# Kernel tuning notes

Measured on AMD Instinct MI355X. Metric: run time of the kernel, lower is better.

The kernel has to match this reference:

```python
import jax, jax.numpy as jnp
import numpy as np

K = 32        # max neighbors per query point
RADIUS = 0.1  # ball radius
N1 = 8192
N2 = 8192


def setup_inputs() -> dict:
    key = jax.random.key(0)
    k1, k2 = jax.random.split(key)
    points1 = jax.random.uniform(k1, (1, N1, 3), dtype=jnp.float32)
    points2 = jax.random.uniform(k2, (1, N2, 3), dtype=jnp.float32)
    lengths1 = jnp.full((1,), N1, dtype=jnp.int32)  # unused by the kernel, kept for API parity
    lengths2 = jnp.full((1,), N2, dtype=jnp.int32)
    return {"points1": points1, "points2": points2, "lengths1": lengths1, "lengths2": lengths2}


def _ball_query(p1, p2, k, radius):
    # p1: [N1,3], p2: [N2,3]
    # squared distances via gram trick, no [N1,N2,3] diff tensor
    d2 = (jnp.sum(p1 * p1, axis=-1)[:, None]
          + jnp.sum(p2 * p2, axis=-1)[None, :]
          - 2.0 * (p1 @ p2.T))                                   # [N1,N2]
    within = d2 <= radius * radius                                # kernel skips only if dist > radius
    n2 = p2.shape[0]
    # pick the first k in-range neighbors in index order (deterministic stand-in
    # for the unspecified hash-grid traversal order)
    score = jnp.where(within, jnp.arange(n2, dtype=jnp.int32), n2)  # [N1,N2]
    _, idx = jax.lax.top_k(-score, k)                             # k smallest scores -> first k indices
    valid = jnp.take_along_axis(within, idx, axis=1)              # [N1,k]
    counts = jnp.minimum(jnp.sum(within, axis=-1), k).astype(jnp.int32)  # [N1]
    mapping = jnp.where(valid, idx, 0).astype(jnp.int32)          # zeros-padded like the torch buffer
    outputs = jnp.where(valid[..., None], p2[mapping], 0.0)       # [N1,k,3]
    return mapping, counts, outputs


def reference(points1, points2, lengths1, lengths2):
    mapping, num_neighbors, outputs = _ball_query(points1[0], points2[0], K, RADIUS)
    return mapping[None], num_neighbors[None], outputs[None]
```

## Files before the change

kernel.cpp:

```cpp
#include <hip/hip_runtime.h>

#define N1 8192
#define N2 8192
#define KNN 32
#define R2_F32 0.009999999776482582f

#define GDIM 10
#define NCELLS (GDIM * GDIM * GDIM)
#define CELL_W 0.109375f
#define INV_W  9.142857142857142f
#define CAP 40
#define HCAP 128
#define PRUNE2 0.0105f

#define WS_CNT 0
#define WS_PTS 4096

__device__ __forceinline__ int cell_coord(float v) {
    int c = (int)(v * INV_W);
    return c > (GDIM - 1) ? (GDIM - 1) : c;
}

__device__ __forceinline__ int prefix_lt(unsigned long long m) {
    return (int)__builtin_amdgcn_mbcnt_hi(
        (unsigned)(m >> 32),
        __builtin_amdgcn_mbcnt_lo((unsigned)m, 0u));
}

__global__ __launch_bounds__(256) void k_scatter(const float* __restrict__ p2,
                                                 int* __restrict__ cnt,
                                                 float4* __restrict__ pts) {
    const int j = (int)(blockIdx.x * blockDim.x + threadIdx.x);
    if (j < N2) {
        const float x = p2[3 * j], y = p2[3 * j + 1], z = p2[3 * j + 2];
        const int c = (cell_coord(x) * GDIM + cell_coord(y)) * GDIM + cell_coord(z);
        const int slot = atomicAdd(&cnt[c], 1);
        if (slot < CAP) pts[c * CAP + slot] = make_float4(x, y, z, (float)j);
    }
}

__global__ __launch_bounds__(256) void k_query(
    const float* __restrict__ p1, const float4* __restrict__ pts,
    const int* __restrict__ cnt,
    float* __restrict__ map_f, float* __restrict__ cnt_f, float* __restrict__ out_f)
{
    __shared__ float4 hits[4][HCAP];
    __shared__ int cum_l[4][32];
    __shared__ int adj_l[4][32];
    const int w    = (int)(threadIdx.x >> 6);
    const int lane = (int)(threadIdx.x & 63);
    const int q    = (int)blockIdx.x * 4 + w;

    const float qx = p1[3 * q], qy = p1[3 * q + 1], qz = p1[3 * q + 2];
    const float s1 = __fadd_rn(__fadd_rn(__fmul_rn(qx, qx), __fmul_rn(qy, qy)),
                               __fmul_rn(qz, qz));

    const int cx = cell_coord(qx), cy = cell_coord(qy), cz = cell_coord(qz);

    int len = 0, id = 0;
    if (lane < 27) {
        const int ax = cx + lane / 9 - 1;
        const int ay = cy + (lane / 3) % 3 - 1;
        const int az = cz + lane % 3 - 1;
        const bool valid = (unsigned)ax < GDIM && (unsigned)ay < GDIM && (unsigned)az < GDIM;
        if (valid) {
            id = (ax * GDIM + ay) * GDIM + az;
            const float gx = fmaxf(0.0f, fmaxf((float)ax * CELL_W - qx, qx - (float)(ax + 1) * CELL_W));
            const float gy = fmaxf(0.0f, fmaxf((float)ay * CELL_W - qy, qy - (float)(ay + 1) * CELL_W));
            const float gz = fmaxf(0.0f, fmaxf((float)az * CELL_W - qz, qz - (float)(az + 1) * CELL_W));
            const float mind2 = gx * gx + gy * gy + gz * gz;
            if (mind2 <= PRUNE2) {
                int c = cnt[id];
                len = c < CAP ? c : CAP;
            }
        }
    }

    int cum = len;
#pragma unroll
    for (int d = 1; d < 32; d <<= 1) {
        const int v = __shfl_up(cum, d, 64);
        if (lane >= d) cum += v;
    }
    const int T = __shfl(cum, 26, 64);
    if (lane < 32) {
        cum_l[w][lane] = cum;
        adj_l[w][lane] = id * CAP - (cum - len);
    }

    int hcnt = 0;
    for (int g0 = 0; g0 < T; g0 += 64) {
        const int g = g0 + lane;
        const bool active = g < T;
        int lo = 0;
#pragma unroll
        for (int st = 16; st > 0; st >>= 1)
            if (cum_l[w][lo + st - 1] <= g) lo += st;
        float4 e = make_float4(2.0f, 2.0f, 2.0f, 0.0f);
        if (active) e = pts[g + adj_l[w][lo]];
        const float s2  = __fadd_rn(__fadd_rn(__fmul_rn(e.x, e.x), __fmul_rn(e.y, e.y)),
                                    __fmul_rn(e.z, e.z));
        const float dot = __fmaf_rn(qz, e.z, __fmaf_rn(qy, e.y, __fmul_rn(qx, e.x)));
        const float d2  = __fsub_rn(__fadd_rn(s1, s2), __fadd_rn(dot, dot));
        const bool within = active && (d2 <= R2_F32);
        const unsigned long long m = __ballot(within);
        if (m) {
            const int pos = hcnt + prefix_lt(m);
            if (within && pos < HCAP) hits[w][pos] = e;
            hcnt += (int)__popcll(m);
        }
    }

    const int cap = hcnt < HCAP ? hcnt : HCAP;
    int k0 = 0x7FFFFFFF, k1 = 0x7FFFFFFF;
    if (lane < cap)      k0 = (((int)hits[w][lane].w) << 7) | lane;
    if (lane + 64 < cap) k1 = (((int)hits[w][lane + 64].w) << 7) | (lane + 64);
    for (int k = 2; k <= 128; k <<= 1) {
        for (int s = k >> 1; s > 0; s >>= 1) {
            if (s == 64) {
                const int lo2 = k0 < k1 ? k0 : k1;
                const int hi2 = k0 < k1 ? k1 : k0;
                k0 = lo2; k1 = hi2;
            } else {
                const int p0 = __shfl_xor(k0, s, 64);
                const int p1 = __shfl_xor(k1, s, 64);
                const bool lower = (lane & s) == 0;
                const bool asc0  = ((lane     ) & k) == 0;
                const bool asc1  = ((lane + 64) & k) == 0;
                k0 = (lower == asc0) ? (k0 < p0 ? k0 : p0) : (k0 > p0 ? k0 : p0);
                k1 = (lower == asc1) ? (k1 < p1 ? k1 : p1) : (k1 > p1 ? k1 : p1);
            }
        }
    }

    const int outc = hcnt < KNN ? hcnt : KNN;
    if (lane < KNN) {
        const int s = q * KNN + lane;
        float* o = out_f + s * 3;
        if (lane < outc) {
            const float4 e = hits[w][k0 & 127];
            map_f[s] = (float)(k0 >> 7);
            o[0] = e.x; o[1] = e.y; o[2] = e.z;
        } else {
            map_f[s] = 0.0f;
            o[0] = 0.0f; o[1] = 0.0f; o[2] = 0.0f;
        }
    }
    if (lane == 0) cnt_f[q] = (float)outc;
}

extern "C" void kernel_launch(void* const* d_in, const int* in_sizes, int n_in,
                              void* d_out, int out_size, void* d_ws, size_t ws_size,
                              hipStream_t stream) {
    const float* p1 = (const float*)d_in[0];
    const float* p2 = (const float*)d_in[1];
    float* out = (float*)d_out;

    float* map_f = out;
    float* cnt_f = out + (size_t)N1 * KNN;
    float* out_f = cnt_f + N1;

    char* ws = (char*)d_ws;
    int*    cnt = (int*)(ws + WS_CNT);
    float4* pts = (float4*)(ws + WS_PTS);

    hipMemsetAsync(cnt, 0, NCELLS * sizeof(int), stream);
    hipLaunchKernelGGL(k_scatter, dim3(N2 / 256), dim3(256), 0, stream, p2, cnt, pts);
    hipLaunchKernelGGL(k_query,   dim3(N1 / 4),   dim3(256), 0, stream,
                       p1, pts, cnt, map_f, cnt_f, out_f);
}
```

Before: 23.76 us.

## Replace atomic scatter and memset with per-cell gather build kernel

Grid construction changes from an atomic scatter over points (which needs a memset first) to one block per cell. Each block scans all of points2 and compacts the points that fall in its cell with ballots, in index order. This drops the memset launch and the atomics, and makes cell contents deterministic and index-ordered. The cost is redundant work: every one of the 1000 blocks reads all 8192 points, about 1000x the global reads of the old scatter, though those reads likely hit in cache.

```diff
diff --git a/kernel.cpp b/kernel.cpp
--- a/kernel.cpp
+++ b/kernel.cpp
@@ -16,6 +16,16 @@
 #define WS_CNT 0
 #define WS_PTS 4096
 
+struct F3 { float x, y, z; };
+
+__device__ __forceinline__ F3 ld3(const float* __restrict__ p, int j) {
+    F3 r;
+    r.x = p[3 * j + 0];
+    r.y = p[3 * j + 1];
+    r.z = p[3 * j + 2];
+    return r;
+}
+
 __device__ __forceinline__ int cell_coord(float v) {
     int c = (int)(v * INV_W);
     return c > (GDIM - 1) ? (GDIM - 1) : c;
@@ -27,16 +37,64 @@
         __builtin_amdgcn_mbcnt_lo((unsigned)m, 0u));
 }
 
-__global__ __launch_bounds__(256) void k_scatter(const float* __restrict__ p2,
-                                                 int* __restrict__ cnt,
-                                                 float4* __restrict__ pts) {
-    const int j = (int)(blockIdx.x * blockDim.x + threadIdx.x);
-    if (j < N2) {
-        const float x = p2[3 * j], y = p2[3 * j + 1], z = p2[3 * j + 2];
-        const int c = (cell_coord(x) * GDIM + cell_coord(y)) * GDIM + cell_coord(z);
-        const int slot = atomicAdd(&cnt[c], 1);
-        if (slot < CAP) pts[c * CAP + slot] = make_float4(x, y, z, (float)j);
-    }
+__global__ __launch_bounds__(256) void k_build(const float* __restrict__ p2,
+                                               int* __restrict__ cnt,
+                                               float4* __restrict__ pts) {
+    __shared__ float4 buf[4][CAP];
+    __shared__ int    cl[4];
+    const int w    = (int)(threadIdx.x >> 6);
+    const int lane = (int)(threadIdx.x & 63);
+    const int c    = (int)blockIdx.x;
+    const int ccx = c / 100, ccy = (c / 10) % 10, ccz = c % 10;
+
+    int count = 0;
+    const int jofs = w * (N2 / 4);
+
+    auto proc = [&](const F3& p, int jb) {
+        const bool match = (cell_coord(p.x) == ccx) &&
+                           (cell_coord(p.y) == ccy) &&
+                           (cell_coord(p.z) == ccz);
+        const unsigned long long m = __ballot(match);
+        if (m) {
+            const int pos = count + prefix_lt(m);
+            if (match && pos < CAP)
+                buf[w][pos] = make_float4(p.x, p.y, p.z, (float)(jb + lane));
+            count += (int)__popcll(m);
+        }
+    };
+
+    constexpr int NMB = (N2 / 4) / 256;
+    F3 b0 = ld3(p2, jofs + 0 * 64 + lane);
+    F3 b1 = ld3(p2, jofs + 1 * 64 + lane);
+    F3 b2 = ld3(p2, jofs + 2 * 64 + lane);
+    F3 b3 = ld3(p2, jofs + 3 * 64 + lane);
+    for (int mb = 0; mb < NMB; ++mb) {
+        const int nb = (mb + 1 < NMB) ? (mb + 1) : 0;
+        F3 n0 = ld3(p2, jofs + nb * 256 + 0 * 64 + lane);
+        F3 n1 = ld3(p2, jofs + nb * 256 + 1 * 64 + lane);
+        F3 n2 = ld3(p2, jofs + nb * 256 + 2 * 64 + lane);
+        F3 n3 = ld3(p2, jofs + nb * 256 + 3 * 64 + lane);
+        const int jb = jofs + mb * 256;
+        proc(b0, jb + 0 * 64);
+        proc(b1, jb + 1 * 64);
+        proc(b2, jb + 2 * 64);
+        proc(b3, jb + 3 * 64);
+        b0 = n0; b1 = n1; b2 = n2; b3 = n3;
+    }
+
+    if (lane == 0) cl[w] = count;
+    __syncthreads();
+
+    const int c0 = cl[0], c1 = cl[1], c2 = cl[2], c3 = cl[3];
+    int start = 0;
+    if (w > 0) start += c0;
+    if (w > 1) start += c1;
+    if (w > 2) start += c2;
+    const int st = start < CAP ? start : CAP;
+    int ns = CAP - st;
+    if (count < ns) ns = count;
+    if (lane < ns) pts[c * CAP + st + lane] = buf[w][lane];
+    if (w == 0 && lane == 0) cnt[c] = c0 + c1 + c2 + c3;
 }
 
 __global__ __launch_bounds__(256) void k_query(
@@ -111,10 +169,10 @@
         }
     }
 
-    const int cap = hcnt < HCAP ? hcnt : HCAP;
+    const int cap2 = hcnt < HCAP ? hcnt : HCAP;
     int k0 = 0x7FFFFFFF, k1 = 0x7FFFFFFF;
-    if (lane < cap)      k0 = (((int)hits[w][lane].w) << 7) | lane;
-    if (lane + 64 < cap) k1 = (((int)hits[w][lane + 64].w) << 7) | (lane + 64);
+    if (lane < cap2)      k0 = (((int)hits[w][lane].w) << 7) | lane;
+    if (lane + 64 < cap2) k1 = (((int)hits[w][lane + 64].w) << 7) | (lane + 64);
     for (int k = 2; k <= 128; k <<= 1) {
         for (int s = k >> 1; s > 0; s >>= 1) {
             if (s == 64) {
@@ -164,8 +222,7 @@
     int*    cnt = (int*)(ws + WS_CNT);
     float4* pts = (float4*)(ws + WS_PTS);
 
-    hipMemsetAsync(cnt, 0, NCELLS * sizeof(int), stream);
-    hipLaunchKernelGGL(k_scatter, dim3(N2 / 256), dim3(256), 0, stream, p2, cnt, pts);
-    hipLaunchKernelGGL(k_query,   dim3(N1 / 4),   dim3(256), 0, stream,
+    hipLaunchKernelGGL(k_build, dim3(NCELLS), dim3(256), 0, stream, p2, cnt, pts);
+    hipLaunchKernelGGL(k_query, dim3(N1 / 4), dim3(256), 0, stream,
                        p1, pts, cnt, map_f, cnt_f, out_f);
 }
```

After: 21.79 us. 1.09x faster.
